# Performance work log

Hardware: AMD Instinct MI355X
Metric: run time of the kernel (lower is better)

## Reference

```python
import jax, jax.numpy as jnp
import numpy as np

B, DIMX, DIMY, DIMH = 256, 128, 128, 128
SMOOTH, CONVEX = 2.0, 1.0
MAX_IT, TOL = 500, 1e-3
sp = jax.nn.softplus


def setup_inputs() -> dict:
    key = jax.random.key(0)
    ks = jax.random.split(key, 32)
    def p(k, *shape):
        # xavier-ish small init for weights/biases
        return (jax.random.normal(k, shape, dtype=jnp.float32) * 0.05)
    return {
        'x': jax.random.normal(ks[0], (B, DIMX), dtype=jnp.float32),
        'y': jax.random.normal(ks[1], (B, DIMY), dtype=jnp.float32),
        # first block (Wuus[0], Wyus[0], Wys[0], Wus[0])
        'wuu0_w': p(ks[2], DIMH, DIMX), 'wuu0_b': p(ks[3], DIMH),
        'wyu0_w': p(ks[4], DIMY, DIMX), 'wyu0_b': p(ks[5], DIMY),
        'wy0': p(ks[6], DIMH, DIMY),
        'wu0_w': p(ks[7], DIMH, DIMX), 'wu0_b': p(ks[8], DIMH),
        # middle block (Wuus[1], Wzus[0], Wzs[0], Wyus[1], Wys[1], Wus[1])
        'wuu1_w': p(ks[9], DIMH, DIMH), 'wuu1_b': p(ks[10], DIMH),
        'wzu1_w': p(ks[11], DIMH, DIMH), 'wzu1_b': p(ks[12], DIMH),
        'wz1': p(ks[13], DIMH, DIMH),
        'wyu1_w': p(ks[14], DIMY, DIMH), 'wyu1_b': p(ks[15], DIMY),
        'wy1': p(ks[16], DIMH, DIMY),
        'wu1_w': p(ks[17], DIMH, DIMH), 'wu1_b': p(ks[18], DIMH),
        # last block (Wzus[-1], Wzs[-1], Wyus[-1], Wys[-1], Wus[-1])
        'wzu2_w': p(ks[19], 1, DIMH), 'wzu2_b': p(ks[20], 1),
        'wz2': p(ks[21], 1, DIMH),
        'wyu2_w': p(ks[22], DIMY, DIMH), 'wyu2_b': p(ks[23], DIMY),
        'wy2': p(ks[24], 1, DIMY),
        'wu2_w': p(ks[25], 1, DIMH), 'wu2_b': p(ks[26], 1),
    }


def reference(x, y, wuu0_w, wuu0_b, wyu0_w, wyu0_b, wy0, wu0_w, wu0_b,
              wuu1_w, wuu1_b, wzu1_w, wzu1_b, wz1, wyu1_w, wyu1_b, wy1, wu1_w, wu1_b,
              wzu2_w, wzu2_b, wz2, wyu2_w, wyu2_b, wy2, wu2_w, wu2_b):
    # ICNN scalar output summed over batch (per-sample outputs decouple in y)
    def icnn_sum(y_):
        u0 = sp(x @ wuu0_w.T + wuu0_b)                                   # [B,H]
        z = sp((y_ * (x @ wyu0_w.T + wyu0_b)) @ wy0.T + x @ wu0_w.T + wu0_b)
        u1 = sp(u0 @ wuu1_w.T + wuu1_b)
        zu = sp(u0 @ wzu1_w.T + wzu1_b)
        z = sp((z * zu) @ jnp.clip(wz1, 0.0, 1e10).T
               + (y_ * (u0 @ wyu1_w.T + wyu1_b)) @ wy1.T
               + u0 @ wu1_w.T + wu1_b)
        zu2 = sp(u1 @ wzu2_w.T + wzu2_b)                                 # [B,1]
        z = ((z * zu2) @ jnp.clip(wz2, 0.0, 1e10).T
             + (y_ * (u1 @ wyu2_w.T + wyu2_b)) @ wy2.T
             + u1 @ wu2_w.T + wu2_b)                                     # [B,1]
        out = z + (0.5 / SMOOTH) * jnp.sum(y_ * y_, axis=1, keepdims=True)
        return jnp.sum(out)

    grad_icnn = jax.grad(icnn_sum)
    step = 2.0 * SMOOTH

    def body(carry, i):
        y1, done = carry
        g = grad_icnn(y1)
        y1_new = y1 + (step / (i + 1.0)) * (y - g)
        conv = jnp.mean(jnp.linalg.norm(y - g, axis=1)) < TOL
        y1 = jnp.where(done, y1, y1_new)  # freeze after 'break'
        return (y1, done | conv), None

    y1_init = jnp.ones_like(y)
    (y1, _), _ = jax.lax.scan(body, (y1_init, jnp.asarray(False)),
                              jnp.arange(MAX_IT, dtype=jnp.float32))
    f_ast1 = y1 + CONVEX * y
    return jnp.mean(f_ast1, axis=1).reshape(-1, 1)
```

## Files before the change

### kernel.cpp

```cpp
#include <hip/hip_runtime.h>
#include <math.h>

#define NB 256
#define N 128
#define NTHREADS 512
#define MAX_IT 500
#define ALF0 0.57126f
#define ALF1 1.81991f
#define ALF2 0.71493f
#define ALF3 1.10956f
#define SLICE 40
#define SLOT(k) ((((k) >> 5) * SLICE) + ((k) & 31))
#define LDSVEC (3 * SLICE + 32)


template <int CTRL>
__device__ __forceinline__ float dpp_add(float p) {
    return p + __int_as_float(__builtin_amdgcn_update_dpp(
                   0, __float_as_int(p), CTRL, 0xF, 0xF, true));
}
__device__ __forceinline__ float quad_sum(float p) {
    p = dpp_add<0xB1>(p);
    p = dpp_add<0x4E>(p);
    return p;
}
__device__ __forceinline__ float wave_sum(float p) {
    p += __shfl_xor(p, 1);
    p += __shfl_xor(p, 2);
    p += __shfl_xor(p, 4);
    p += __shfl_xor(p, 8);
    p += __shfl_xor(p, 16);
    p += __shfl_xor(p, 32);
    return p;
}
__device__ __forceinline__ float softplus_f(float s) {
    float e = __expf(-fabsf(s));
    return fmaxf(s, 0.f) + __logf(1.f + e);
}
__device__ __forceinline__ float sigmoid_f(float s) {
    float e = __expf(-fabsf(s));
    float r = 1.f / (1.f + e);
    return s >= 0.f ? r : 1.f - r;
}

__device__ __forceinline__ float mv_row(const float* __restrict__ W,
                                        const float* __restrict__ V,
                                        int k, int h) {
    const float4* wr = (const float4*)(W + k * N + h * 32);
    const float4* vr = (const float4*)(V + h * SLICE);
    float q0 = 0.f, q1 = 0.f, q2 = 0.f, q3 = 0.f;
#pragma unroll
    for (int i = 0; i < 8; ++i) {
        float4 w = wr[i], v = vr[i];
        q0 = fmaf(w.x, v.x, q0); q1 = fmaf(w.y, v.y, q1);
        q2 = fmaf(w.z, v.z, q2); q3 = fmaf(w.w, v.w, q3);
    }
    return quad_sum((q0 + q1) + (q2 + q3));
}

__global__ __launch_bounds__(NTHREADS, 2)
void picnn_solve(const float* __restrict__ x, const float* __restrict__ y,
                 const float* __restrict__ wuu0_w, const float* __restrict__ wuu0_b,
                 const float* __restrict__ wyu0_w, const float* __restrict__ wyu0_b,
                 const float* __restrict__ wy0,
                 const float* __restrict__ wu0_w, const float* __restrict__ wu0_b,
                 const float* __restrict__ wuu1_w, const float* __restrict__ wuu1_b,
                 const float* __restrict__ wzu1_w, const float* __restrict__ wzu1_b,
                 const float* __restrict__ wz1,
                 const float* __restrict__ wyu1_w, const float* __restrict__ wyu1_b,
                 const float* __restrict__ wy1,
                 const float* __restrict__ wu1_w, const float* __restrict__ wu1_b,
                 const float* __restrict__ wzu2_w, const float* __restrict__ wzu2_b,
                 const float* __restrict__ wz2,
                 const float* __restrict__ wyu2_w, const float* __restrict__ wyu2_b,
                 const float* __restrict__ wy2,
                 float* __restrict__ out)
{
    const int b = blockIdx.x;
    const int t = threadIdx.x;
    const int k = t >> 2;
    const int h = t & 3;
    const int wave = t >> 6;
    const int lane = t & 63;

    __shared__ __align__(16) float xv[LDSVEC];
    __shared__ __align__(16) float u0v[LDSVEC];
    __shared__ __align__(16) float u1v[LDSVEC];
    __shared__ __align__(16) float t0s[LDSVEC];
    __shared__ __align__(16) float t2s[LDSVEC];
    __shared__ __align__(16) float t1s[LDSVEC];
    __shared__ __align__(16) float d2s[LDSVEC];
    __shared__ __align__(16) float d1s[LDSVEC];
    __shared__ float rp[8];
    __shared__ __align__(16) float4 img1[8 * NTHREADS];
    __shared__ __align__(16) float4 img2[8 * NTHREADS];

    if (t < N) xv[SLOT(t)] = x[b * N + t];
    __syncthreads();

    float u0k = softplus_f(mv_row(wuu0_w, xv, k, h) + wuu0_b[k]);
    float a0  = mv_row(wyu0_w, xv, k, h) + wyu0_b[k];
    float c0  = mv_row(wu0_w,  xv, k, h) + wu0_b[k];
    if (h == 0) u0v[SLOT(k)] = u0k;
    __syncthreads();

    float u1k = softplus_f(mv_row(wuu1_w, u0v, k, h) + wuu1_b[k]);
    float zu  = softplus_f(mv_row(wzu1_w, u0v, k, h) + wzu1_b[k]);
    float a1  = mv_row(wyu1_w, u0v, k, h) + wyu1_b[k];
    float c1  = mv_row(wu1_w,  u0v, k, h) + wu1_b[k];
    if (h == 0) u1v[SLOT(k)] = u1k;
    __syncthreads();

    float a2 = mv_row(wyu2_w, u1v, k, h) + wyu2_b[k];
    float e2 = a2 * wy2[k];
    float dp;
    {
        const float4* wr = (const float4*)(wzu2_w + h * 32);
        const float4* vr = (const float4*)(u1v + h * SLICE);
        float q0 = 0.f, q1 = 0.f, q2 = 0.f, q3 = 0.f;
#pragma unroll
        for (int i = 0; i < 8; ++i) {
            float4 w = wr[i], v = vr[i];
            q0 = fmaf(w.x, v.x, q0); q1 = fmaf(w.y, v.y, q1);
            q2 = fmaf(w.z, v.z, q2); q3 = fmaf(w.w, v.w, q3);
        }
        float zu2 = softplus_f(quad_sum((q0 + q1) + (q2 + q3)) + wzu2_b[0]);
        dp = zu2 * fmaxf(wz2[k], 0.f);
    }

    float4 wf0[8], wf1[8], wf2[8];
    float4 wb0[8];
    {
        const float4* r0 = (const float4*)(wy0 + k * N + h * 32);
        const float4* r1 = (const float4*)(wz1 + k * N + h * 32);
        const float4* r2 = (const float4*)(wy1 + k * N + h * 32);
#pragma unroll
        for (int i = 0; i < 8; ++i) {
            wf0[i] = r0[i];
            float4 z = r1[i];
            z.x = fmaxf(z.x, 0.f); z.y = fmaxf(z.y, 0.f);
            z.z = fmaxf(z.z, 0.f); z.w = fmaxf(z.w, 0.f);
            wf1[i] = z;
            wf2[i] = r2[i];
        }
#pragma unroll
        for (int i = 0; i < 8; ++i) {
            int r = h * 32 + 4 * i;
            wb0[i].x = wy0[(r + 0) * N + k]; wb0[i].y = wy0[(r + 1) * N + k];
            wb0[i].z = wy0[(r + 2) * N + k]; wb0[i].w = wy0[(r + 3) * N + k];
            float4 z1c, c1c;
            z1c.x = fmaxf(wz1[(r + 0) * N + k], 0.f);
            z1c.y = fmaxf(wz1[(r + 1) * N + k], 0.f);
            z1c.z = fmaxf(wz1[(r + 2) * N + k], 0.f);
            z1c.w = fmaxf(wz1[(r + 3) * N + k], 0.f);
            img1[i * NTHREADS + t] = z1c;
            c1c.x = wy1[(r + 0) * N + k]; c1c.y = wy1[(r + 1) * N + k];
            c1c.z = wy1[(r + 2) * N + k]; c1c.w = wy1[(r + 3) * N + k];
            img2[i * NTHREADS + t] = c1c;
        }
    }

    const float yk = y[b * N + k];
    float y1v = 2.f * (yk - e2);
    if (h == 0) { t0s[SLOT(k)] = y1v * a0; t2s[SLOT(k)] = y1v * a1; }
    __syncthreads();

    for (int it = 1; it <= MAX_IT; ++it) {
        const float4* t0r = (const float4*)(t0s + h * SLICE);
        const float4* t2r = (const float4*)(t2s + h * SLICE);
        float p0 = 0.f, p1 = 0.f, p2 = 0.f, p3 = 0.f;
        float q0 = 0.f, q1 = 0.f, q2 = 0.f, q3 = 0.f;
#pragma unroll
        for (int i = 0; i < 8; ++i) {
            float4 v0 = t0r[i], v2 = t2r[i];
            p0 = fmaf(wf0[i].x, v0.x, p0); p1 = fmaf(wf0[i].y, v0.y, p1);
            p2 = fmaf(wf0[i].z, v0.z, p2); p3 = fmaf(wf0[i].w, v0.w, p3);
            q0 = fmaf(wf2[i].x, v2.x, q0); q1 = fmaf(wf2[i].y, v2.y, q1);
            q2 = fmaf(wf2[i].z, v2.z, q2); q3 = fmaf(wf2[i].w, v2.w, q3);
        }
        float s1  = quad_sum((p0 + p1) + (p2 + p3)) + c0;
        float s2a = quad_sum((q0 + q1) + (q2 + q3));
        float e1 = __expf(-fabsf(s1));
        float z1 = fmaxf(s1, 0.f) + __logf(1.f + e1);
        float rr1 = 1.f / (1.f + e1);
        float sig1 = (s1 >= 0.f) ? rr1 : 1.f - rr1;
        if (h == 0) t1s[SLOT(k)] = z1 * zu;
        __syncthreads();

        const float4* t1r = (const float4*)(t1s + h * SLICE);
        p0 = p1 = p2 = p3 = 0.f;
#pragma unroll
        for (int i = 0; i < 8; ++i) {
            float4 v1 = t1r[i];
            p0 = fmaf(wf1[i].x, v1.x, p0); p1 = fmaf(wf1[i].y, v1.y, p1);
            p2 = fmaf(wf1[i].z, v1.z, p2); p3 = fmaf(wf1[i].w, v1.w, p3);
        }
        float s2 = quad_sum((p0 + p1) + (p2 + p3)) + s2a + c1;
        float d2 = dp * sigmoid_f(s2);
        if (h == 0) d2s[SLOT(k)] = d2;
        __syncthreads();

        const float4* d2r = (const float4*)(d2s + h * SLICE);
        p0 = p1 = p2 = p3 = 0.f; q0 = q1 = q2 = q3 = 0.f;
#pragma unroll
        for (int i = 0; i < 8; ++i) {
            float4 d = d2r[i];
            float4 w1 = img1[i * NTHREADS + t];
            float4 w2 = img2[i * NTHREADS + t];
            p0 = fmaf(w1.x, d.x, p0); p1 = fmaf(w1.y, d.y, p1);
            p2 = fmaf(w1.z, d.z, p2); p3 = fmaf(w1.w, d.w, p3);
            q0 = fmaf(w2.x, d.x, q0); q1 = fmaf(w2.y, d.y, q1);
            q2 = fmaf(w2.z, d.z, q2); q3 = fmaf(w2.w, d.w, q3);
        }
        float qv = quad_sum((p0 + p1) + (p2 + p3));
        float gc = quad_sum((q0 + q1) + (q2 + q3));
        float d1 = qv * zu * sig1;
        if (h == 0) d1s[SLOT(k)] = d1;
        __syncthreads();

        const float4* d1r = (const float4*)(d1s + h * SLICE);
        p0 = p1 = p2 = p3 = 0.f;
#pragma unroll
        for (int i = 0; i < 8; ++i) {
            float4 d = d1r[i];
            p0 = fmaf(wb0[i].x, d.x, p0); p1 = fmaf(wb0[i].y, d.y, p1);
            p2 = fmaf(wb0[i].z, d.z, p2); p3 = fmaf(wb0[i].w, d.w, p3);
        }
        float gb = quad_sum((p0 + p1) + (p2 + p3));
        float g = fmaf(0.5f, y1v, e2) + gc * a1 + gb * a0;
        float rres = yk - g;
        int ph = (it - 1) & 3;
        float alf = (ph == 0) ? ALF0 : (ph == 1) ? ALF1
                  : (ph == 2) ? ALF2 : ALF3;
        y1v = fmaf(alf, rres, y1v);
        if (h == 0) { t0s[SLOT(k)] = y1v * a0; t2s[SLOT(k)] = y1v * a1; }
        float rs = wave_sum(rres * rres);
        if (lane == 0) rp[wave] = rs;
        __syncthreads();
        float tot = ((rp[0] + rp[1]) + (rp[2] + rp[3]))
                  + ((rp[4] + rp[5]) + (rp[6] + rp[7]));
        if (tot < 4e-6f) break;
    }

    __syncthreads();
    float v = wave_sum(y1v + yk);
    if (lane == 0) rp[wave] = v;
    __syncthreads();
    if (t == 0) {
        float s = ((rp[0] + rp[1]) + (rp[2] + rp[3]))
                + ((rp[4] + rp[5]) + (rp[6] + rp[7]));
        out[b] = s * (1.f / 512.f);
    }
}

extern "C" void kernel_launch(void* const* d_in, const int* in_sizes, int n_in,
                              void* d_out, int out_size, void* d_ws, size_t ws_size,
                              hipStream_t stream) {
    const float* x      = (const float*)d_in[0];
    const float* y      = (const float*)d_in[1];
    const float* wuu0_w = (const float*)d_in[2];
    const float* wuu0_b = (const float*)d_in[3];
    const float* wyu0_w = (const float*)d_in[4];
    const float* wyu0_b = (const float*)d_in[5];
    const float* wy0    = (const float*)d_in[6];
    const float* wu0_w  = (const float*)d_in[7];
    const float* wu0_b  = (const float*)d_in[8];
    const float* wuu1_w = (const float*)d_in[9];
    const float* wuu1_b = (const float*)d_in[10];
    const float* wzu1_w = (const float*)d_in[11];
    const float* wzu1_b = (const float*)d_in[12];
    const float* wz1    = (const float*)d_in[13];
    const float* wyu1_w = (const float*)d_in[14];
    const float* wyu1_b = (const float*)d_in[15];
    const float* wy1    = (const float*)d_in[16];
    const float* wu1_w  = (const float*)d_in[17];
    const float* wu1_b  = (const float*)d_in[18];
    const float* wzu2_w = (const float*)d_in[19];
    const float* wzu2_b = (const float*)d_in[20];
    const float* wz2    = (const float*)d_in[21];
    const float* wyu2_w = (const float*)d_in[22];
    const float* wyu2_b = (const float*)d_in[23];
    const float* wy2    = (const float*)d_in[24];
    float* out = (float*)d_out;

    picnn_solve<<<dim3(NB), dim3(NTHREADS), 0, stream>>>(
        x, y, wuu0_w, wuu0_b, wyu0_w, wyu0_b, wy0, wu0_w, wu0_b,
        wuu1_w, wuu1_b, wzu1_w, wzu1_b, wz1, wyu1_w, wyu1_b, wy1, wu1_w, wu1_b,
        wzu2_w, wzu2_b, wz2, wyu2_w, wyu2_b, wy2, out);
}
```

Baseline: 150.0 us.

## Fold a0/a1 scaling into weights, share y1 vector, defer convergence check

Pre-scales the wy0 and wy1 weight registers and their transposed LDS images by the per-row a0/a1 activations. The loop can then broadcast a single y1 vector through LDS instead of two scaled vectors, and the gradient no longer needs multiplies by a0/a1. The residual reduction now uses DPP row adds plus two shuffles instead of six shuffles. The convergence test reads the partial sums at the start of the next iteration, overlapping it with the LDS loads. This changes floating-point rounding order slightly, and the stored partials must still be valid when read after the barrier.

```diff
diff --git a/kernel.cpp b/kernel.cpp
--- a/kernel.cpp
+++ b/kernel.cpp
@@ -22,6 +22,12 @@
 __device__ __forceinline__ float quad_sum(float p) {
     p = dpp_add<0xB1>(p);
     p = dpp_add<0x4E>(p);
+    return p;
+}
+__device__ __forceinline__ float row_sum16(float p) {
+    p = quad_sum(p);
+    p = dpp_add<0x124>(p);
+    p = dpp_add<0x128>(p);
     return p;
 }
 __device__ __forceinline__ float wave_sum(float p) {
@@ -86,8 +92,9 @@
     __shared__ __align__(16) float xv[LDSVEC];
     __shared__ __align__(16) float u0v[LDSVEC];
     __shared__ __align__(16) float u1v[LDSVEC];
-    __shared__ __align__(16) float t0s[LDSVEC];
-    __shared__ __align__(16) float t2s[LDSVEC];
+    __shared__ __align__(16) float a0s[LDSVEC];
+    __shared__ __align__(16) float a1s[LDSVEC];
+    __shared__ __align__(16) float y1s[LDSVEC];
     __shared__ __align__(16) float t1s[LDSVEC];
     __shared__ __align__(16) float d2s[LDSVEC];
     __shared__ __align__(16) float d1s[LDSVEC];
@@ -99,20 +106,19 @@
     __syncthreads();
 
     float u0k = softplus_f(mv_row(wuu0_w, xv, k, h) + wuu0_b[k]);
-    float a0  = mv_row(wyu0_w, xv, k, h) + wyu0_b[k];
+    float a0k = mv_row(wyu0_w, xv, k, h) + wyu0_b[k];
     float c0  = mv_row(wu0_w,  xv, k, h) + wu0_b[k];
-    if (h == 0) u0v[SLOT(k)] = u0k;
+    if (h == 0) { u0v[SLOT(k)] = u0k; a0s[SLOT(k)] = a0k; }
     __syncthreads();
 
     float u1k = softplus_f(mv_row(wuu1_w, u0v, k, h) + wuu1_b[k]);
     float zu  = softplus_f(mv_row(wzu1_w, u0v, k, h) + wzu1_b[k]);
-    float a1  = mv_row(wyu1_w, u0v, k, h) + wyu1_b[k];
+    float a1k = mv_row(wyu1_w, u0v, k, h) + wyu1_b[k];
     float c1  = mv_row(wu1_w,  u0v, k, h) + wu1_b[k];
-    if (h == 0) u1v[SLOT(k)] = u1k;
+    if (h == 0) { u1v[SLOT(k)] = u1k; a1s[SLOT(k)] = a1k; }
     __syncthreads();
 
     float a2 = mv_row(wyu2_w, u1v, k, h) + wyu2_b[k];
-    float e2 = a2 * wy2[k];
     float dp;
     {
         const float4* wr = (const float4*)(wzu2_w + h * 32);
@@ -134,49 +140,69 @@
         const float4* r0 = (const float4*)(wy0 + k * N + h * 32);
         const float4* r1 = (const float4*)(wz1 + k * N + h * 32);
         const float4* r2 = (const float4*)(wy1 + k * N + h * 32);
-#pragma unroll
-        for (int i = 0; i < 8; ++i) {
-            wf0[i] = r0[i];
+        const float4* a0r = (const float4*)(a0s + h * SLICE);
+        const float4* a1r = (const float4*)(a1s + h * SLICE);
+#pragma unroll
+        for (int i = 0; i < 8; ++i) {
+            float4 a = r0[i], s0 = a0r[i];
+            a.x *= s0.x; a.y *= s0.y; a.z *= s0.z; a.w *= s0.w;
+            wf0[i] = a;
             float4 z = r1[i];
             z.x = fmaxf(z.x, 0.f); z.y = fmaxf(z.y, 0.f);
             z.z = fmaxf(z.z, 0.f); z.w = fmaxf(z.w, 0.f);
             wf1[i] = z;
-            wf2[i] = r2[i];
+            float4 c = r2[i], s1 = a1r[i];
+            c.x *= s1.x; c.y *= s1.y; c.z *= s1.z; c.w *= s1.w;
+            wf2[i] = c;
         }
 #pragma unroll
         for (int i = 0; i < 8; ++i) {
             int r = h * 32 + 4 * i;
-            wb0[i].x = wy0[(r + 0) * N + k]; wb0[i].y = wy0[(r + 1) * N + k];
-            wb0[i].z = wy0[(r + 2) * N + k]; wb0[i].w = wy0[(r + 3) * N + k];
+            wb0[i].x = wy0[(r + 0) * N + k] * a0k;
+            wb0[i].y = wy0[(r + 1) * N + k] * a0k;
+            wb0[i].z = wy0[(r + 2) * N + k] * a0k;
+            wb0[i].w = wy0[(r + 3) * N + k] * a0k;
             float4 z1c, c1c;
             z1c.x = fmaxf(wz1[(r + 0) * N + k], 0.f);
             z1c.y = fmaxf(wz1[(r + 1) * N + k], 0.f);
             z1c.z = fmaxf(wz1[(r + 2) * N + k], 0.f);
             z1c.w = fmaxf(wz1[(r + 3) * N + k], 0.f);
             img1[i * NTHREADS + t] = z1c;
-            c1c.x = wy1[(r + 0) * N + k]; c1c.y = wy1[(r + 1) * N + k];
-            c1c.z = wy1[(r + 2) * N + k]; c1c.w = wy1[(r + 3) * N + k];
+            c1c.x = wy1[(r + 0) * N + k] * a1k;
+            c1c.y = wy1[(r + 1) * N + k] * a1k;
+            c1c.z = wy1[(r + 2) * N + k] * a1k;
+            c1c.w = wy1[(r + 3) * N + k] * a1k;
             img2[i * NTHREADS + t] = c1c;
         }
     }
 
     const float yk = y[b * N + k];
-    float y1v = 2.f * (yk - e2);
-    if (h == 0) { t0s[SLOT(k)] = y1v * a0; t2s[SLOT(k)] = y1v * a1; }
+    const float ye2 = yk - a2 * wy2[k];
+    float y1v = 2.f * ye2;
+    if (h == 0) y1s[SLOT(k)] = y1v;
     __syncthreads();
 
     for (int it = 1; it <= MAX_IT; ++it) {
-        const float4* t0r = (const float4*)(t0s + h * SLICE);
-        const float4* t2r = (const float4*)(t2s + h * SLICE);
+        const float4* yr = (const float4*)(y1s + h * SLICE);
+        float4 vv[8];
+#pragma unroll
+        for (int i = 0; i < 8; ++i) vv[i] = yr[i];
+        if (it > 1) {
+            const float4* rpv = (const float4*)rp;
+            float4 ua = rpv[0], ub = rpv[1];
+            float4 u = ua + ub;
+            float tot = (u.x + u.y) + (u.z + u.w);
+            if (tot < 4e-6f) break;
+        }
         float p0 = 0.f, p1 = 0.f, p2 = 0.f, p3 = 0.f;
         float q0 = 0.f, q1 = 0.f, q2 = 0.f, q3 = 0.f;
 #pragma unroll
         for (int i = 0; i < 8; ++i) {
-            float4 v0 = t0r[i], v2 = t2r[i];
-            p0 = fmaf(wf0[i].x, v0.x, p0); p1 = fmaf(wf0[i].y, v0.y, p1);
-            p2 = fmaf(wf0[i].z, v0.z, p2); p3 = fmaf(wf0[i].w, v0.w, p3);
-            q0 = fmaf(wf2[i].x, v2.x, q0); q1 = fmaf(wf2[i].y, v2.y, q1);
-            q2 = fmaf(wf2[i].z, v2.z, q2); q3 = fmaf(wf2[i].w, v2.w, q3);
+            float4 v = vv[i];
+            p0 = fmaf(wf0[i].x, v.x, p0); p1 = fmaf(wf0[i].y, v.y, p1);
+            p2 = fmaf(wf0[i].z, v.z, p2); p3 = fmaf(wf0[i].w, v.w, p3);
+            q0 = fmaf(wf2[i].x, v.x, q0); q1 = fmaf(wf2[i].y, v.y, q1);
+            q2 = fmaf(wf2[i].z, v.z, q2); q3 = fmaf(wf2[i].w, v.w, q3);
         }
         float s1  = quad_sum((p0 + p1) + (p2 + p3)) + c0;
         float s2a = quad_sum((q0 + q1) + (q2 + q3));
@@ -212,8 +238,8 @@
             q0 = fmaf(w2.x, d.x, q0); q1 = fmaf(w2.y, d.y, q1);
             q2 = fmaf(w2.z, d.z, q2); q3 = fmaf(w2.w, d.w, q3);
         }
-        float qv = quad_sum((p0 + p1) + (p2 + p3));
-        float gc = quad_sum((q0 + q1) + (q2 + q3));
+        float qv  = quad_sum((p0 + p1) + (p2 + p3));
+        float gcp = quad_sum((q0 + q1) + (q2 + q3));
         float d1 = qv * zu * sig1;
         if (h == 0) d1s[SLOT(k)] = d1;
         __syncthreads();
@@ -226,20 +252,18 @@
             p0 = fmaf(wb0[i].x, d.x, p0); p1 = fmaf(wb0[i].y, d.y, p1);
             p2 = fmaf(wb0[i].z, d.z, p2); p3 = fmaf(wb0[i].w, d.w, p3);
         }
-        float gb = quad_sum((p0 + p1) + (p2 + p3));
-        float g = fmaf(0.5f, y1v, e2) + gc * a1 + gb * a0;
-        float rres = yk - g;
+        float gbp = quad_sum((p0 + p1) + (p2 + p3));
+        float rres = ye2 - fmaf(0.5f, y1v, gcp + gbp);
         int ph = (it - 1) & 3;
         float alf = (ph == 0) ? ALF0 : (ph == 1) ? ALF1
                   : (ph == 2) ? ALF2 : ALF3;
         y1v = fmaf(alf, rres, y1v);
-        if (h == 0) { t0s[SLOT(k)] = y1v * a0; t2s[SLOT(k)] = y1v * a1; }
-        float rs = wave_sum(rres * rres);
+        if (h == 0) y1s[SLOT(k)] = y1v;
+        float rs = row_sum16(rres * rres);
+        rs += __shfl_xor(rs, 16);
+        rs += __shfl_xor(rs, 32);
         if (lane == 0) rp[wave] = rs;
         __syncthreads();
-        float tot = ((rp[0] + rp[1]) + (rp[2] + rp[3]))
-                  + ((rp[4] + rp[5]) + (rp[6] + rp[7]));
-        if (tot < 4e-6f) break;
     }
 
     __syncthreads();
```

Result: faster. 145.8 us, median of 2 (-2.8%).
